# Performance work log

Measured on AMD Instinct MI355X. Metric: run time of the kernel, lower is better.

## Reference

```python
import jax, jax.numpy as jnp
import numpy as np

B, T = 8, 1024
C_IN, C_H = 4096, 4096
K_I, K_H = 3, 3
INIT_SPARSITY = 0.15


def _fixed_fanin_bipartite(rng, n_out, n_in, k):
    # exactly k True entries per row, distinct columns
    r = rng.random((n_out, n_in))
    cols = np.argsort(r, axis=1)[:, :k]
    A = np.zeros((n_out, n_in), np.float32)
    np.put_along_axis(A, cols, 1.0, axis=1)
    return A


def _fixed_fanin_graph(rng, n, k):
    # exactly k True entries per row, distinct non-self columns
    r = rng.random((n, n))
    np.fill_diagonal(r, 2.0)  # exclude self-loops
    cols = np.argsort(r, axis=1)[:, :k]
    A = np.zeros((n, n), np.float32)
    np.put_along_axis(A, cols, 1.0, axis=1)
    return A


def setup_inputs() -> dict:
    rng = np.random.default_rng(0)
    z = jnp.asarray(rng.random((B, T, C_IN)) < INIT_SPARSITY)          # bool (B,T,C_in)
    h0 = jnp.asarray(rng.random((B, C_H)) < INIT_SPARSITY)             # bool (B,C_h)
    A_input_f = jnp.asarray(_fixed_fanin_bipartite(rng, C_H, C_IN, K_I))  # (C_h,C_in) f32
    A_hidden_f = jnp.asarray(_fixed_fanin_graph(rng, C_H, K_H))           # (C_h,C_h) f32
    return {"z": z, "h0": h0, "A_input_f": A_input_f, "A_hidden_f": A_hidden_f}


def reference(z, h0, A_input_f, A_hidden_f):
    # AND-of-ORs CA: h_i(t) = [OR over input fan-in of z(t)] AND [OR over hidden fan-in of h(t-1)]
    z_tf = jnp.moveaxis(z, -2, 0)  # (T, B, C_in)

    def step(h, z_t):
        input_or = (z_t.astype(jnp.float32) @ A_input_f.T) > 0   # (B, C_h) bool
        hidden_or = (h.astype(jnp.float32) @ A_hidden_f.T) > 0   # (B, C_h) bool
        h_new = input_or & hidden_or
        return h_new, h_new

    _, h_seq = jax.lax.scan(step, h0, z_tf)   # (T, B, C_h)
    h_seq = jnp.moveaxis(h_seq, 0, -2)        # (B, T, C_h)
    return jnp.concatenate([z, h_seq], axis=-1)  # (B, T, C_in + C_h) bool
```

## Files before the change

### kernel.cpp

```cpp
#include <hip/hip_runtime.h>
#include <stdint.h>

#define B_   8
#define T_   1024
#define CIN_ 4096
#define CH_  4096
#define GRP  16
#define NGRP (T_ / GRP)
#define NCOPY 512


__device__ __forceinline__ uint32_t bytes_nonzero01(uint32_t w) {
  uint32_t t = (w & 0x7F7F7F7Fu) + 0x7F7F7F7Fu;
  t = (t | w) & 0x80808080u;
  return t >> 7;
}

__device__ __forceinline__ uint32_t load4(const void* base, long idx4, int es) {
  if (es == 1) {
    uint32_t w = ((const uint32_t*)base)[idx4];
    return bytes_nonzero01(w);
  } else if (es == 2) {
    uint32_t w0 = ((const uint32_t*)base)[idx4 * 2];
    uint32_t w1 = ((const uint32_t*)base)[idx4 * 2 + 1];
    uint32_t r = 0;
    r |= ((w0 & 0xFFFFu) != 0u) ? 0x00000001u : 0u;
    r |= ((w0 >> 16)     != 0u) ? 0x00000100u : 0u;
    r |= ((w1 & 0xFFFFu) != 0u) ? 0x00010000u : 0u;
    r |= ((w1 >> 16)     != 0u) ? 0x01000000u : 0u;
    return r;
  } else {
    uint4 w = ((const uint4*)base)[idx4];
    uint32_t r = 0;
    r |= (w.x != 0u) ? 0x00000001u : 0u;
    r |= (w.y != 0u) ? 0x00000100u : 0u;
    r |= (w.z != 0u) ? 0x00010000u : 0u;
    r |= (w.w != 0u) ? 0x01000000u : 0u;
    return r;
  }
}

__device__ __forceinline__ uint4 expand01(uint32_t v4) {
  uint4 r = { v4 & 1u, (v4 >> 8) & 1u, (v4 >> 16) & 1u, (v4 >> 24) & 1u };
  return r;
}

__global__ __launch_bounds__(256) void extract_kernel(const float* __restrict__ Ain,
                                                      const float* __restrict__ Ah,
                                                      uint32_t* __restrict__ idxin,
                                                      uint32_t* __restrict__ idxh,
                                                      const uint32_t* __restrict__ z,
                                                      uint32_t* __restrict__ modep) {
  if (blockIdx.x == 2048) {
    __shared__ int sB, sH, sW, sL;
    const int n = threadIdx.x;
    if (n == 0) { sB = 1; sH = 1; sW = 1; sL = 0; }
    __syncthreads();
    int okB = 1, okH = 1, okW = 1, low = 0;
    for (int k = 0; k < 16; ++k) {
      uint32_t w = z[n + 256 * k];
      if ((w & 0xFEFEFEFEu) != 0u) okB = 0;
      uint32_t lo = w & 0xFFFFu, hi = w >> 16;
      if (!((lo == 0u || lo == 0x3F80u) && (hi == 0u || hi == 0x3F80u))) okH = 0;
      if (!(w == 0u || w == 1u)) okW = 0;
      if (lo != 0u) low = 1;
    }
    if (!okB) atomicAnd(&sB, 0);
    if (!okH) atomicAnd(&sH, 0);
    if (!okW) atomicAnd(&sW, 0);
    if (low)  atomicOr(&sL, 1);
    __syncthreads();
    if (n == 0) {
      uint32_t mode;
      if (sW)      mode = 4;
      else if (sB) mode = 1;
      else if (sH) mode = sL ? 2 : 4;
      else         mode = 1;
      modep[0] = mode;
    }
    return;
  }
  const int wave = threadIdx.x >> 6;
  const int lane = threadIdx.x & 63;
  const int row  = blockIdx.x * 4 + wave;
  const float* A;
  uint32_t* outp;
  if (row < 4096) { A = Ain + (long)row * 4096;          outp = idxin + row * 3; }
  else            { A = Ah  + (long)(row - 4096) * 4096; outp = idxh + (row - 4096) * 3; }
  __shared__ int cnt[4];
  if (lane == 0) cnt[wave] = 0;
  __syncthreads();
  const float4* A4 = (const float4*)A;
  #pragma unroll
  for (int it = 0; it < 16; ++it) {
    float4 v = A4[it * 64 + lane];
    int cbase = (it * 64 + lane) * 4;
    if (v.x != 0.0f) { int q = atomicAdd(&cnt[wave], 1); if (q < 3) outp[q] = cbase;     }
    if (v.y != 0.0f) { int q = atomicAdd(&cnt[wave], 1); if (q < 3) outp[q] = cbase + 1; }
    if (v.z != 0.0f) { int q = atomicAdd(&cnt[wave], 1); if (q < 3) outp[q] = cbase + 2; }
    if (v.w != 0.0f) { int q = atomicAdd(&cnt[wave], 1); if (q < 3) outp[q] = cbase + 3; }
  }
}

__global__ __launch_bounds__(1024) void inor_kernel(const void* __restrict__ z,
                                                    const uint32_t* __restrict__ idxin,
                                                    const uint32_t* __restrict__ modep,
                                                    uint32_t* __restrict__ in_orb) {
  const int t = blockIdx.x;
  const int n = threadIdx.x;
  const int es = (int)modep[0];
  __shared__ __align__(16) unsigned char zp[4096];
  uint32_t acc = 0;
  #pragma unroll
  for (int b = 0; b < B_; ++b)
    acc |= load4(z, ((long)b * T_ + t) * 1024 + n, es) << b;
  ((uint32_t*)zp)[n] = acc;
  __syncthreads();
  const uint4* ip = (const uint4*)(idxin + n * 12);
  uint4 q0 = ip[0], q1 = ip[1], q2 = ip[2];
  uint32_t r0 = (uint32_t)zp[q0.x] | zp[q0.y] | zp[q0.z];
  uint32_t r1 = (uint32_t)zp[q0.w] | zp[q1.x] | zp[q1.y];
  uint32_t r2 = (uint32_t)zp[q1.z] | zp[q1.w] | zp[q2.x];
  uint32_t r3 = (uint32_t)zp[q2.y] | zp[q2.z] | zp[q2.w];
  in_orb[t * 1024 + n] = r0 | (r1 << 8) | (r2 << 16) | (r3 << 24);
}

__global__ __launch_bounds__(1024) void scan_copy_kernel(const uint32_t* __restrict__ in_orb,
                                                         const uint32_t* __restrict__ idxh,
                                                         const void* __restrict__ h0,
                                                         const void* __restrict__ z,
                                                         const uint32_t* __restrict__ modep,
                                                         uint32_t* __restrict__ out) {
  const int n = threadIdx.x;
  const int es = (int)modep[0];

  if (blockIdx.x >= 8) {
    const long total4 = (long)B_ * T_ * 1024;
    const long stride = (long)NCOPY * 1024;
    uint4* out4 = (uint4*)out;
    for (long i4 = (long)(blockIdx.x - 8) * 1024 + n; i4 < total4; i4 += stride) {
      uint32_t v = load4(z, i4, es);
      long row = i4 >> 10, c4 = i4 & 1023;
      out4[row * 2048 + c4] = expand01(v);
    }
    return;
  }

  __builtin_amdgcn_s_setprio(1);
  __shared__ __align__(16) unsigned char smem[88 * 1024];
  unsigned char* hb0 = &smem[0];
  unsigned char* hb1 = &smem[4096];
  uint32_t* stg = (uint32_t*)&smem[8192];
  const int b = blockIdx.x;

  uint32_t d[4][3];
  {
    const uint4* p = (const uint4*)(idxh + n * 12);
    uint4 q0 = p[0], q1 = p[1], q2 = p[2];
    d[0][0] = q0.x; d[0][1] = q0.y; d[0][2] = q0.z;
    d[1][0] = q0.w; d[1][1] = q1.x; d[1][2] = q1.y;
    d[2][0] = q1.z; d[2][1] = q1.w; d[2][2] = q2.x;
    d[3][0] = q2.y; d[3][1] = q2.z; d[3][2] = q2.w;
  }
  ((uint32_t*)hb0)[n] = load4(h0, (long)b * 1024 + n, es);
  uint32_t* outh = out + (long)b * T_ * 8192 + 4096;

  for (int g = 0; g < NGRP; ++g) {
    {
      const uint4* src = (const uint4*)(in_orb + g * (GRP * 1024));
      uint4 s0 = src[n], s1 = src[n + 1024], s2 = src[n + 2048], s3 = src[n + 3072];
      uint4* dst = (uint4*)stg;
      dst[n] = s0; dst[n + 1024] = s1; dst[n + 2048] = s2; dst[n + 3072] = s3;
    }
    __syncthreads();

    uint32_t oacc[GRP];
    #pragma unroll
    for (int tt = 0; tt < GRP; ++tt) {
      const unsigned char* hc = (tt & 1) ? hb1 : hb0;
      unsigned char* hn = (tt & 1) ? hb0 : hb1;
      uint32_t inw = stg[tt * 1024 + n];
      uint32_t mask = (inw >> b) & 0x01010101u;
      uint32_t o4 = 0;
      if (mask) {
        if (mask & 0x00000001u) { uint32_t v = (uint32_t)hc[d[0][0]] | hc[d[0][1]] | hc[d[0][2]]; o4 |= v; }
        if (mask & 0x00000100u) { uint32_t v = (uint32_t)hc[d[1][0]] | hc[d[1][1]] | hc[d[1][2]]; o4 |= v << 8; }
        if (mask & 0x00010000u) { uint32_t v = (uint32_t)hc[d[2][0]] | hc[d[2][1]] | hc[d[2][2]]; o4 |= v << 16; }
        if (mask & 0x01000000u) { uint32_t v = (uint32_t)hc[d[3][0]] | hc[d[3][1]] | hc[d[3][2]]; o4 |= v << 24; }
      }
      ((uint32_t*)hn)[n] = o4;
      oacc[tt] = o4;
      __syncthreads();
    }

    #pragma unroll
    for (int tt = 0; tt < GRP; ++tt)
      ((uint4*)(outh + (long)(g * GRP + tt) * 8192))[n] = expand01(oacc[tt]);
  }
}

extern "C" void kernel_launch(void* const* d_in, const int* in_sizes, int n_in,
                              void* d_out, int out_size, void* d_ws, size_t ws_size,
                              hipStream_t stream) {
  const void*  z   = d_in[0];
  const void*  h0  = d_in[1];
  const float* Ain = (const float*)d_in[2];
  const float* Ah  = (const float*)d_in[3];
  uint32_t* out = (uint32_t*)d_out;

  char* ws = (char*)d_ws;
  uint32_t* modep = (uint32_t*)(ws);
  uint32_t* idxin = (uint32_t*)(ws + 256);
  uint32_t* idxh  = (uint32_t*)(ws + 256 + 49152);
  uint32_t* inorb = (uint32_t*)(ws + 98560);

  extract_kernel  <<<2049, 256,  0, stream>>>(Ain, Ah, idxin, idxh,
                                              (const uint32_t*)z, modep);
  inor_kernel     <<<T_,   1024, 0, stream>>>(z, idxin, modep, inorb);
  scan_copy_kernel<<<8 + NCOPY, 1024, 0, stream>>>(inorb, idxh, h0, z, modep, out);
}
```

Before: 1.173 ms.

## Fuse input-OR into scan kernel with flag handoff and move z copy to prep

Merges the input-OR kernel into the scan kernel. Extra blocks compute per-timestep input-OR words and signal completion through per-group atomic counters. The 8 scan blocks spin-wait on those flags and prefetch the next group into registers rather than staging through shared memory. The z-to-output copy moves into the prep kernel as extra blocks. This removes one launch and overlaps input-OR with the serial scan, but the scan now depends on the producer blocks being scheduled, and the register prefetch raises register pressure.

```diff
diff --git a/kernel.cpp b/kernel.cpp
--- a/kernel.cpp
+++ b/kernel.cpp
@@ -7,7 +7,8 @@
 #define CH_  4096
 #define GRP  16
 #define NGRP (T_ / GRP)
-#define NCOPY 512
+
+#define F_INOR 8
 
 
 __device__ __forceinline__ uint32_t bytes_nonzero01(uint32_t w) {
@@ -45,49 +46,75 @@
   return r;
 }
 
-__global__ __launch_bounds__(256) void extract_kernel(const float* __restrict__ Ain,
-                                                      const float* __restrict__ Ah,
-                                                      uint32_t* __restrict__ idxin,
-                                                      uint32_t* __restrict__ idxh,
-                                                      const uint32_t* __restrict__ z,
-                                                      uint32_t* __restrict__ modep) {
-  if (blockIdx.x == 2048) {
-    __shared__ int sB, sH, sW, sL;
-    const int n = threadIdx.x;
-    if (n == 0) { sB = 1; sH = 1; sW = 1; sL = 0; }
+__device__ __forceinline__ void wait_ge(uint32_t* p, uint32_t tgt) {
+  while (__hip_atomic_load(p, __ATOMIC_RELAXED, __HIP_MEMORY_SCOPE_AGENT) < tgt)
+    __builtin_amdgcn_s_sleep(2);
+  __threadfence();
+}
+__device__ __forceinline__ void bump(uint32_t* p) {
+  __threadfence();
+  __hip_atomic_fetch_add(p, 1u, __ATOMIC_RELAXED, __HIP_MEMORY_SCOPE_AGENT);
+}
+
+__global__ __launch_bounds__(256) void prep_kernel(const float* __restrict__ Ain,
+                                                   const float* __restrict__ Ah,
+                                                   uint32_t* __restrict__ idxin,
+                                                   uint32_t* __restrict__ idxh,
+                                                   const void* __restrict__ z,
+                                                   uint32_t* __restrict__ modep,
+                                                   uint32_t* __restrict__ flags,
+                                                   uint32_t* __restrict__ out) {
+  __shared__ int cnt[4];
+  const int n = threadIdx.x;
+  const uint32_t* zw = (const uint32_t*)z;
+
+  if (blockIdx.x == 2048 || blockIdx.x > 2048) {
+    if (n == 0) { cnt[0] = 1; cnt[1] = 1; cnt[2] = 1; cnt[3] = 0; }
     __syncthreads();
     int okB = 1, okH = 1, okW = 1, low = 0;
     for (int k = 0; k < 16; ++k) {
-      uint32_t w = z[n + 256 * k];
+      uint32_t w = zw[n + 256 * k];
       if ((w & 0xFEFEFEFEu) != 0u) okB = 0;
       uint32_t lo = w & 0xFFFFu, hi = w >> 16;
       if (!((lo == 0u || lo == 0x3F80u) && (hi == 0u || hi == 0x3F80u))) okH = 0;
       if (!(w == 0u || w == 1u)) okW = 0;
       if (lo != 0u) low = 1;
     }
-    if (!okB) atomicAnd(&sB, 0);
-    if (!okH) atomicAnd(&sH, 0);
-    if (!okW) atomicAnd(&sW, 0);
-    if (low)  atomicOr(&sL, 1);
-    __syncthreads();
-    if (n == 0) {
-      uint32_t mode;
-      if (sW)      mode = 4;
-      else if (sB) mode = 1;
-      else if (sH) mode = sL ? 2 : 4;
-      else         mode = 1;
-      modep[0] = mode;
+    if (!okB) atomicAnd(&cnt[0], 0);
+    if (!okH) atomicAnd(&cnt[1], 0);
+    if (!okW) atomicAnd(&cnt[2], 0);
+    if (low)  atomicOr(&cnt[3], 1);
+    __syncthreads();
+    uint32_t mode;
+    if (cnt[2])      mode = 4;
+    else if (cnt[0]) mode = 1;
+    else if (cnt[1]) mode = cnt[3] ? 2 : 4;
+    else             mode = 1;
+
+    if (blockIdx.x == 2048) {
+      if (n == 0) modep[0] = mode;
+      if (n < 128) flags[n] = 0;
+      return;
+    }
+    const int es = (int)mode;
+    uint4* out4 = (uint4*)out;
+    long i4 = (long)(blockIdx.x - 2049) * 256 + n;
+    #pragma unroll 4
+    for (int k = 0; k < 32; ++k, i4 += 262144) {
+      uint32_t v = load4(z, i4, es);
+      long row = i4 >> 10, c4 = i4 & 1023;
+      out4[row * 2048 + c4] = expand01(v);
     }
     return;
   }
-  const int wave = threadIdx.x >> 6;
-  const int lane = threadIdx.x & 63;
+
+  const int wave = n >> 6;
+  const int lane = n & 63;
   const int row  = blockIdx.x * 4 + wave;
   const float* A;
   uint32_t* outp;
   if (row < 4096) { A = Ain + (long)row * 4096;          outp = idxin + row * 3; }
   else            { A = Ah  + (long)(row - 4096) * 4096; outp = idxh + (row - 4096) * 3; }
-  __shared__ int cnt[4];
   if (lane == 0) cnt[wave] = 0;
   __syncthreads();
   const float4* A4 = (const float4*)A;
@@ -102,56 +129,43 @@
   }
 }
 
-__global__ __launch_bounds__(1024) void inor_kernel(const void* __restrict__ z,
-                                                    const uint32_t* __restrict__ idxin,
-                                                    const uint32_t* __restrict__ modep,
-                                                    uint32_t* __restrict__ in_orb) {
-  const int t = blockIdx.x;
-  const int n = threadIdx.x;
-  const int es = (int)modep[0];
-  __shared__ __align__(16) unsigned char zp[4096];
-  uint32_t acc = 0;
-  #pragma unroll
-  for (int b = 0; b < B_; ++b)
-    acc |= load4(z, ((long)b * T_ + t) * 1024 + n, es) << b;
-  ((uint32_t*)zp)[n] = acc;
-  __syncthreads();
-  const uint4* ip = (const uint4*)(idxin + n * 12);
-  uint4 q0 = ip[0], q1 = ip[1], q2 = ip[2];
-  uint32_t r0 = (uint32_t)zp[q0.x] | zp[q0.y] | zp[q0.z];
-  uint32_t r1 = (uint32_t)zp[q0.w] | zp[q1.x] | zp[q1.y];
-  uint32_t r2 = (uint32_t)zp[q1.z] | zp[q1.w] | zp[q2.x];
-  uint32_t r3 = (uint32_t)zp[q2.y] | zp[q2.z] | zp[q2.w];
-  in_orb[t * 1024 + n] = r0 | (r1 << 8) | (r2 << 16) | (r3 << 24);
-}
-
-__global__ __launch_bounds__(1024) void scan_copy_kernel(const uint32_t* __restrict__ in_orb,
+__global__ __launch_bounds__(1024) void scan_inor_kernel(const void* __restrict__ z,
+                                                         const void* __restrict__ h0,
+                                                         const uint32_t* __restrict__ modep,
+                                                         const uint32_t* __restrict__ idxin,
                                                          const uint32_t* __restrict__ idxh,
-                                                         const void* __restrict__ h0,
-                                                         const void* __restrict__ z,
-                                                         const uint32_t* __restrict__ modep,
+                                                         uint32_t* __restrict__ inorb,
+                                                         uint32_t* __restrict__ flags,
                                                          uint32_t* __restrict__ out) {
-  const int n = threadIdx.x;
-  const int es = (int)modep[0];
-
-  if (blockIdx.x >= 8) {
-    const long total4 = (long)B_ * T_ * 1024;
-    const long stride = (long)NCOPY * 1024;
-    uint4* out4 = (uint4*)out;
-    for (long i4 = (long)(blockIdx.x - 8) * 1024 + n; i4 < total4; i4 += stride) {
-      uint32_t v = load4(z, i4, es);
-      long row = i4 >> 10, c4 = i4 & 1023;
-      out4[row * 2048 + c4] = expand01(v);
-    }
-    return;
-  }
-
-  __builtin_amdgcn_s_setprio(1);
   __shared__ __align__(16) unsigned char smem[88 * 1024];
   unsigned char* hb0 = &smem[0];
   unsigned char* hb1 = &smem[4096];
-  uint32_t* stg = (uint32_t*)&smem[8192];
-  const int b = blockIdx.x;
+  const int n = threadIdx.x;
+  const int es = (int)modep[0];
+
+  if (blockIdx.x >= 8) {
+    const int t = (int)blockIdx.x - 8;
+    uint32_t acc = 0;
+    #pragma unroll
+    for (int b = 0; b < B_; ++b)
+      acc |= load4(z, ((long)b * T_ + t) * 1024 + n, es) << b;
+    ((uint32_t*)hb0)[n] = acc;
+    __syncthreads();
+    const unsigned char* zp = hb0;
+    const uint4* ip = (const uint4*)(idxin + n * 12);
+    uint4 q0 = ip[0], q1 = ip[1], q2 = ip[2];
+    uint32_t r0 = (uint32_t)zp[q0.x] | zp[q0.y] | zp[q0.z];
+    uint32_t r1 = (uint32_t)zp[q0.w] | zp[q1.x] | zp[q1.y];
+    uint32_t r2 = (uint32_t)zp[q1.z] | zp[q1.w] | zp[q2.x];
+    uint32_t r3 = (uint32_t)zp[q2.y] | zp[q2.z] | zp[q2.w];
+    inorb[t * 1024 + n] = r0 | (r1 << 8) | (r2 << 16) | (r3 << 24);
+    __syncthreads();
+    if (n == 0) bump(&flags[F_INOR + (t >> 4)]);
+    return;
+  }
+
+  __builtin_amdgcn_s_setprio(1);
+  const int b = (int)blockIdx.x;
 
   uint32_t d[4][3];
   {
@@ -165,22 +179,24 @@
   ((uint32_t*)hb0)[n] = load4(h0, (long)b * 1024 + n, es);
   uint32_t* outh = out + (long)b * T_ * 8192 + 4096;
 
+  if (n == 0) wait_ge(&flags[F_INOR + 0], GRP);
+  __syncthreads();
+  uint32_t cur[GRP], nxt[GRP], oacc[GRP];
+  #pragma unroll
+  for (int i = 0; i < GRP; ++i) cur[i] = inorb[i * 1024 + n];
+
   for (int g = 0; g < NGRP; ++g) {
-    {
-      const uint4* src = (const uint4*)(in_orb + g * (GRP * 1024));
-      uint4 s0 = src[n], s1 = src[n + 1024], s2 = src[n + 2048], s3 = src[n + 3072];
-      uint4* dst = (uint4*)stg;
-      dst[n] = s0; dst[n + 1024] = s1; dst[n + 2048] = s2; dst[n + 3072] = s3;
-    }
-    __syncthreads();
-
-    uint32_t oacc[GRP];
+    if (g + 1 < NGRP) {
+      if (n == 0) wait_ge(&flags[F_INOR + g + 1], GRP);
+      __syncthreads();
+      #pragma unroll
+      for (int i = 0; i < GRP; ++i) nxt[i] = inorb[((g + 1) * GRP + i) * 1024 + n];
+    }
     #pragma unroll
     for (int tt = 0; tt < GRP; ++tt) {
       const unsigned char* hc = (tt & 1) ? hb1 : hb0;
       unsigned char* hn = (tt & 1) ? hb0 : hb1;
-      uint32_t inw = stg[tt * 1024 + n];
-      uint32_t mask = (inw >> b) & 0x01010101u;
+      uint32_t mask = (cur[tt] >> b) & 0x01010101u;
       uint32_t o4 = 0;
       if (mask) {
         if (mask & 0x00000001u) { uint32_t v = (uint32_t)hc[d[0][0]] | hc[d[0][1]] | hc[d[0][2]]; o4 |= v; }
@@ -192,10 +208,11 @@
       oacc[tt] = o4;
       __syncthreads();
     }
-
     #pragma unroll
     for (int tt = 0; tt < GRP; ++tt)
       ((uint4*)(outh + (long)(g * GRP + tt) * 8192))[n] = expand01(oacc[tt]);
+    #pragma unroll
+    for (int i = 0; i < GRP; ++i) cur[i] = nxt[i];
   }
 }
 
@@ -213,9 +230,10 @@
   uint32_t* idxin = (uint32_t*)(ws + 256);
   uint32_t* idxh  = (uint32_t*)(ws + 256 + 49152);
   uint32_t* inorb = (uint32_t*)(ws + 98560);
-
-  extract_kernel  <<<2049, 256,  0, stream>>>(Ain, Ah, idxin, idxh,
-                                              (const uint32_t*)z, modep);
-  inor_kernel     <<<T_,   1024, 0, stream>>>(z, idxin, modep, inorb);
-  scan_copy_kernel<<<8 + NCOPY, 1024, 0, stream>>>(inorb, idxh, h0, z, modep, out);
-}
+  uint32_t* flagp = (uint32_t*)(ws + 4292864);
+
+  prep_kernel     <<<3073, 256,  0, stream>>>(Ain, Ah, idxin, idxh, z,
+                                              modep, flagp, out);
+  scan_inor_kernel<<<8 + T_, 1024, 0, stream>>>(z, h0, modep, idxin, idxh,
+                                                inorb, flagp, out);
+}
```

Result: faster. 1.091 ms (-7.0%).
